# Kernel tuning notes

Hardware: AMD Instinct MI355X
Metric: run time of the kernel (lower is better)

## Reference

```python
import jax, jax.numpy as jnp
from jax import lax
import numpy as np

T, B, I, H, O = 512, 32, 512, 512, 512


def _gru_layer(x_seq, h0, w_ih, w_hh, b_ih, b_hh, reverse):
    """Single-direction GRU layer, PyTorch gate semantics (r,z,n order).
    x_seq: (T,B,in), h0: (B,H). Returns ys:(T,B,H) in original time order, hT:(B,H)."""
    gi = jnp.einsum('tbi,gi->tbg', x_seq, w_ih) + b_ih  # (T,B,3H) input gates precomputed

    def step(h, gi_t):
        gh = h @ w_hh.T + b_hh
        ir, iz, i_n = jnp.split(gi_t, 3, axis=-1)
        hr, hz, hn = jnp.split(gh, 3, axis=-1)
        r = jax.nn.sigmoid(ir + hr)
        z = jax.nn.sigmoid(iz + hz)
        n = jnp.tanh(i_n + r * hn)
        h_new = (1.0 - z) * n + z * h
        return h_new, h_new

    hT, ys = lax.scan(step, h0, gi, reverse=reverse)
    return ys, hT


def setup_inputs() -> dict:
    key = jax.random.key(0)
    ks = jax.random.split(key, 20)
    s = 1.0 / np.sqrt(H)
    u = lambda k, shape: jax.random.uniform(k, shape, jnp.float32, -s, s)
    inp = {
        'x': jax.random.normal(ks[0], (T, B, I), jnp.float32),
        'h': jnp.zeros((4, B, H), jnp.float32),
        # layer 0 (input I), forward/backward
        'w_ih_0f': u(ks[1], (3 * H, I)), 'w_hh_0f': u(ks[2], (3 * H, H)),
        'b_ih_0f': u(ks[3], (3 * H,)),   'b_hh_0f': u(ks[4], (3 * H,)),
        'w_ih_0b': u(ks[5], (3 * H, I)), 'w_hh_0b': u(ks[6], (3 * H, H)),
        'b_ih_0b': u(ks[7], (3 * H,)),   'b_hh_0b': u(ks[8], (3 * H,)),
        # layer 1 (input 2H)
        'w_ih_1f': u(ks[9], (3 * H, 2 * H)), 'w_hh_1f': u(ks[10], (3 * H, H)),
        'b_ih_1f': u(ks[11], (3 * H,)),      'b_hh_1f': u(ks[12], (3 * H,)),
        'w_ih_1b': u(ks[13], (3 * H, 2 * H)), 'w_hh_1b': u(ks[14], (3 * H, H)),
        'b_ih_1b': u(ks[15], (3 * H,)),       'b_hh_1b': u(ks[16], (3 * H,)),
        # final linear: (O, 2H)
        'fc_w': u(ks[17], (O, 2 * H)), 'fc_b': u(ks[18], (O,)),
    }
    return inp


def reference(x, h,
              w_ih_0f, w_hh_0f, b_ih_0f, b_hh_0f,
              w_ih_0b, w_hh_0b, b_ih_0b, b_hh_0b,
              w_ih_1f, w_hh_1f, b_ih_1f, b_hh_1f,
              w_ih_1b, w_hh_1b, b_ih_1b, b_hh_1b,
              fc_w, fc_b):
    # layer 0: h indices 0 (fwd), 1 (bwd)
    y0f, h0f = _gru_layer(x, h[0], w_ih_0f, w_hh_0f, b_ih_0f, b_hh_0f, reverse=False)
    y0b, h0b = _gru_layer(x, h[1], w_ih_0b, w_hh_0b, b_ih_0b, b_hh_0b, reverse=True)
    x1 = jnp.concatenate([y0f, y0b], axis=-1)  # (T,B,2H)
    # layer 1: h indices 2 (fwd), 3 (bwd)
    y1f, h1f = _gru_layer(x1, h[2], w_ih_1f, w_hh_1f, b_ih_1f, b_hh_1f, reverse=False)
    y1b, h1b = _gru_layer(x1, h[3], w_ih_1b, w_hh_1b, b_ih_1b, b_hh_1b, reverse=True)
    out = jnp.concatenate([y1f, y1b], axis=-1)  # (T,B,2H)
    out = jnp.einsum('tbh,oh->tbo', out, fc_w) + fc_b
    h_n = jnp.stack([h0f, h0b, h1f, h1b], axis=0)  # (4,B,H)
    return out, h_n
```

## Files before the change

### kernel.cpp

```cpp
#include <hip/hip_runtime.h>


typedef unsigned short u16;
typedef __attribute__((ext_vector_type(8))) short bf16x8;
typedef __attribute__((ext_vector_type(4))) float f32x4;

__device__ __forceinline__ u16 f2bf(float f) {
  unsigned u = __float_as_uint(f);
  u += 0x7fffu + ((u >> 16) & 1u);
  return (u16)(u >> 16);
}
__device__ __forceinline__ float bf2f(unsigned v) {
  return __uint_as_float(v << 16);
}
__device__ __forceinline__ float frcp(float x) {
  float r;
  asm("v_rcp_f32 %0, %1" : "=v"(r) : "v"(x));
  return r;
}

template<int AUX>
__device__ __forceinline__ void gl_lds16(const void* g, void* l) {
  __builtin_amdgcn_global_load_lds((const __attribute__((address_space(1))) void*)g,
                                   (__attribute__((address_space(3))) void*)l, 16, 0, AUX);
}

__device__ __forceinline__ void st_u64_sc0(void* p, uint2 v) {
  asm volatile("global_store_dwordx2 %0, %1, off sc0" :: "v"(p), "v"(v) : "memory");
}
__device__ __forceinline__ unsigned atom_rd_l2(unsigned* p) {
  unsigned r;
  asm volatile("global_atomic_add %0, %1, %2, off sc0\n\ts_waitcnt vmcnt(0)"
               : "=v"(r) : "v"(p), "v"(0u) : "memory");
  return r;
}
__device__ __forceinline__ void atom_add_l2(unsigned* p, unsigned v) {
  asm volatile("global_atomic_add %0, %1, off" :: "v"(p), "v"(v) : "memory");
}


__global__ void k_zero(unsigned* p, int n) {
  int i = blockIdx.x * blockDim.x + threadIdx.x;
  if (i < n) p[i] = 0u;
}

__global__ void k_cvt(const float* __restrict__ s, u16* __restrict__ d, int n) {
  int i = (blockIdx.x * blockDim.x + threadIdx.x) * 4;
  if (i < n) {
    float4 v = *(const float4*)(s + i);
    unsigned a = (unsigned)f2bf(v.x) | ((unsigned)f2bf(v.y) << 16);
    unsigned b = (unsigned)f2bf(v.z) | ((unsigned)f2bf(v.w) << 16);
    uint2 o; o.x = a; o.y = b;
    *(uint2*)(d + i) = o;
  }
}

__global__ void k_copyf(const float* __restrict__ s, float* __restrict__ d, int n) {
  int i = blockIdx.x * blockDim.x + threadIdx.x;
  if (i < n) d[i] = s[i];
}


template<bool BF16OUT>
__global__ __launch_bounds__(256) void k_gemm(
    const u16* __restrict__ A, const u16* __restrict__ B,
    const float* __restrict__ bias, void* __restrict__ Cv,
    int N, int K)
{
  __shared__ u16 As[128 * 32];
  __shared__ u16 Bs[128 * 32];
  const int tid = threadIdx.x;
  const int w = tid >> 6, l = tid & 63;
  const int bm = blockIdx.x, bn = blockIdx.y;
  const int lj = l & 15, lk = l >> 4;
  const int wm = (w & 1) * 64, wn = (w >> 1) * 64;
  const int srow = l >> 2, scol = (l & 3) * 8;
  f32x4 acc[4][4] = {};
  const u16* Ab = A + (size_t)bm * 128 * K;
  const u16* Bb = B + (size_t)bn * 128 * K;

  for (int kt = 0; kt < K; kt += 32) {
#pragma unroll
    for (int i = 0; i < 2; ++i) {
      int r0 = i * 64 + w * 16;
      gl_lds16<0>(Ab + (size_t)(r0 + srow) * K + kt + scol, &As[r0 * 32]);
      gl_lds16<0>(Bb + (size_t)(r0 + srow) * K + kt + scol, &Bs[r0 * 32]);
    }
    __syncthreads();
    bf16x8 af[4], bf[4];
#pragma unroll
    for (int i = 0; i < 4; ++i) af[i] = *(const bf16x8*)&As[(wm + i * 16 + lj) * 32 + lk * 8];
#pragma unroll
    for (int j = 0; j < 4; ++j) bf[j] = *(const bf16x8*)&Bs[(wn + j * 16 + lj) * 32 + lk * 8];
#pragma unroll
    for (int i = 0; i < 4; ++i)
#pragma unroll
      for (int j = 0; j < 4; ++j)
        acc[i][j] = __builtin_amdgcn_mfma_f32_16x16x32_bf16(af[i], bf[j], acc[i][j], 0, 0, 0);
    __syncthreads();
  }

#pragma unroll
  for (int i = 0; i < 4; ++i)
#pragma unroll
    for (int j = 0; j < 4; ++j) {
      int col = bn * 128 + wn + j * 16 + lj;
      float bv = bias[col];
#pragma unroll
      for (int r2 = 0; r2 < 4; ++r2) {
        int row = bm * 128 + wm + i * 16 + lk * 4 + r2;
        float v = acc[i][j][r2] + bv;
        if (BF16OUT) ((u16*)Cv)[(size_t)row * N + col] = f2bf(v);
        else         ((float*)Cv)[(size_t)row * N + col] = v;
      }
    }
}


#define LSTR 536

__global__ __launch_bounds__(256, 1) void k_gru(
    const u16*  __restrict__ gi,
    const float* __restrict__ whhf,
    const float* __restrict__ whhb,
    const float* __restrict__ bhhf,
    const float* __restrict__ bhhb,
    const float* __restrict__ h0,
    const u16*  __restrict__ hinit,
    u16* __restrict__ y,
    float* __restrict__ hn,
    unsigned* __restrict__ cnt,
    unsigned* __restrict__ elect)
{
  __shared__ u16 hl[2][32 * LSTR];
  __shared__ int sh_role;
  __shared__ int sh_go;
  const int tid = threadIdx.x;

  if (tid == 0) {
    sh_go = -1;
    unsigned xcc;
    asm volatile("s_getreg_b32 %0, hwreg(HW_REG_XCC_ID)" : "=s"(xcc));
    xcc &= 7u;
    unsigned t = __hip_atomic_fetch_add(&elect[xcc], 1u, __ATOMIC_RELAXED,
                                        __HIP_MEMORY_SCOPE_AGENT);
    int role = -1;
    if (t < 16u) {
      if (t == 15u) {
        unsigned expected = 0u;
        __hip_atomic_compare_exchange_strong(&elect[8], &expected, xcc + 1u,
            __ATOMIC_RELAXED, __ATOMIC_RELAXED, __HIP_MEMORY_SCOPE_AGENT);
      }
      unsigned cap = 0;
      for (;;) {
        unsigned wv = __hip_atomic_load(&elect[8], __ATOMIC_RELAXED,
                                        __HIP_MEMORY_SCOPE_AGENT);
        if (wv != 0u) { if (wv == xcc + 1u) role = (int)t; break; }
        if (++cap > (1u << 22)) break;
        __builtin_amdgcn_s_sleep(2);
      }
    }
    sh_role = role;
  }
  __syncthreads();
  const int role = sh_role;
  if (role < 0) return;

  const int w = tid >> 6, l = tid & 63;
  const int dir = w >> 1, p = w & 1;
  const int j0 = role * 32 + p * 16;
  const int lj = l & 15, lk = l >> 4;
  const float* whh = dir ? whhb : whhf;
  const float* bhh = dir ? bhhb : bhhf;
  volatile int* go_v = (volatile int*)&sh_go;

  bf16x8 bfr[3][16];
#pragma unroll
  for (int g = 0; g < 3; ++g) {
    const float* wr = whh + (size_t)(g * 512 + j0 + lj) * 512;
#pragma unroll
    for (int kc = 0; kc < 16; ++kc) {
      const float* s4 = wr + kc * 32 + lk * 8;
      float4 a = *(const float4*)s4;
      float4 b = *(const float4*)(s4 + 4);
      bf16x8 v;
      v[0] = (short)f2bf(a.x); v[1] = (short)f2bf(a.y); v[2] = (short)f2bf(a.z); v[3] = (short)f2bf(a.w);
      v[4] = (short)f2bf(b.x); v[5] = (short)f2bf(b.y); v[6] = (short)f2bf(b.z); v[7] = (short)f2bf(b.w);
      bfr[g][kc] = v;
    }
  }
  f32x4 bbv[3];
#pragma unroll
  for (int g = 0; g < 3; ++g)
    bbv[g] = *(const f32x4*)&bhh[g * 512 + j0 + lk * 4];

  float hreg[2][4];
#pragma unroll
  for (int bt = 0; bt < 2; ++bt) {
    f32x4 hv = *(const f32x4*)&h0[((size_t)dir * 32 + bt * 16 + lj) * 512 + j0 + lk * 4];
#pragma unroll
    for (int r = 0; r < 4; ++r) hreg[bt][r] = hv[r];
  }

  uint2 guc[2][3];
  {
    const int tq0 = dir ? 511 : 0;
#pragma unroll
    for (int bt = 0; bt < 2; ++bt)
#pragma unroll
      for (int g = 0; g < 3; ++g)
        guc[bt][g] = *(const uint2*)(gi + ((size_t)tq0 * 32 + bt * 16 + lj) * 3072
                                     + dir * 1536 + g * 512 + j0 + lk * 4);
  }

  for (int s = 0; s < 512; ++s) {
    const int tq = dir ? (511 - s) : s;

    if (s > 0) {
      if (w == 0) {
        const unsigned target = 4u * (unsigned)s;
        unsigned cap = 0;
        for (;;) {
          unsigned v = 0xFFFFFFFFu;
          if (l < 4) v = atom_rd_l2(cnt + (l << 5));
          if (__all((int)((l < 4) ? (v >= target) : 1))) break;
          if (++cap > (1u << 14)) break;
        }
        if (l == 0) *go_v = s;
      } else {
        unsigned cap = 0;
        while (*go_v < s) { if (++cap > (1u << 20)) break; }
      }
    }

    {
      const u16* src; int rstride, cbase;
      if (s == 0) { src = hinit + (size_t)dir * 32 * 512; rstride = 512; cbase = 0; }
      else { int tp = dir ? (tq + 1) : (tq - 1); src = y + (size_t)tp * 32 * 1024; rstride = 1024; cbase = dir * 512; }
#pragma unroll
      for (int r = 0; r < 16; ++r) {
        int row = p * 16 + r;
        gl_lds16<1>(src + (size_t)row * rstride + cbase + l * 8, &hl[dir][row * LSTR]);
      }
    }
    asm volatile("s_waitcnt vmcnt(0)" ::: "memory");
    __syncthreads();

    uint2 gun[2][3];
    {
      const int sq = (s < 511) ? (s + 1) : 511;
      const int tqn = dir ? (511 - sq) : sq;
#pragma unroll
      for (int bt = 0; bt < 2; ++bt)
#pragma unroll
        for (int g = 0; g < 3; ++g)
          gun[bt][g] = *(const uint2*)(gi + ((size_t)tqn * 32 + bt * 16 + lj) * 3072
                                       + dir * 1536 + g * 512 + j0 + lk * 4);
    }

    f32x4 acc[2][3];
#pragma unroll
    for (int bt = 0; bt < 2; ++bt)
#pragma unroll
      for (int g = 0; g < 3; ++g)
        acc[bt][g] = bbv[g];

#pragma unroll
    for (int kc = 0; kc < 16; ++kc) {
      bf16x8 a0 = *(const bf16x8*)&hl[dir][lj * LSTR + kc * 32 + lk * 8];
      bf16x8 a1 = *(const bf16x8*)&hl[dir][(16 + lj) * LSTR + kc * 32 + lk * 8];
#pragma unroll
      for (int g = 0; g < 3; ++g) {
        acc[0][g] = __builtin_amdgcn_mfma_f32_16x16x32_bf16(bfr[g][kc], a0, acc[0][g], 0, 0, 0);
        acc[1][g] = __builtin_amdgcn_mfma_f32_16x16x32_bf16(bfr[g][kc], a1, acc[1][g], 0, 0, 0);
      }
    }

#pragma unroll
    for (int bt = 0; bt < 2; ++bt) {
      const int b = bt * 16 + lj;
      unsigned q[4];
      float hv[4];
#pragma unroll
      for (int r = 0; r < 4; ++r) {
        unsigned w0 = (r & 1) ? (((const unsigned*)&guc[bt][0])[r >> 1] >> 16)
                              : (((const unsigned*)&guc[bt][0])[r >> 1] & 0xffffu);
        unsigned w1 = (r & 1) ? (((const unsigned*)&guc[bt][1])[r >> 1] >> 16)
                              : (((const unsigned*)&guc[bt][1])[r >> 1] & 0xffffu);
        unsigned w2 = (r & 1) ? (((const unsigned*)&guc[bt][2])[r >> 1] >> 16)
                              : (((const unsigned*)&guc[bt][2])[r >> 1] & 0xffffu);
        float rr = frcp(1.f + __expf(-(bf2f(w0) + acc[bt][0][r])));
        float zz = frcp(1.f + __expf(-(bf2f(w1) + acc[bt][1][r])));
        float nx = bf2f(w2) + rr * acc[bt][2][r];
        float nn = 1.f - 2.f * frcp(1.f + __expf(2.f * nx));
        float h = (1.f - zz) * nn + zz * hreg[bt][r];
        hreg[bt][r] = h;
        hv[r] = h;
        q[r] = (unsigned)f2bf(h);
      }
      uint2 pack; pack.x = q[0] | (q[1] << 16); pack.y = q[2] | (q[3] << 16);
      st_u64_sc0(y + ((size_t)tq * 32 + b) * 1024 + dir * 512 + j0 + lk * 4, pack);
      if (s == 511) {
        float4 o; o.x = hv[0]; o.y = hv[1]; o.z = hv[2]; o.w = hv[3];
        *(float4*)&hn[((size_t)dir * 32 + b) * 512 + j0 + lk * 4] = o;
      }
    }

#pragma unroll
    for (int bt = 0; bt < 2; ++bt)
#pragma unroll
      for (int g = 0; g < 3; ++g)
        guc[bt][g] = gun[bt][g];

    asm volatile("s_waitcnt vmcnt(0)" ::: "memory");
    __syncthreads();
    if (tid == 0) atom_add_l2(cnt + ((role & 3) << 5), 1u);
  }
}


extern "C" void kernel_launch(void* const* d_in, const int* in_sizes, int n_in,
                              void* d_out, int out_size, void* d_ws, size_t ws_size,
                              hipStream_t stream)
{
  const float* x     = (const float*)d_in[0];
  const float* h     = (const float*)d_in[1];
  const float* wih0f = (const float*)d_in[2];
  const float* whh0f = (const float*)d_in[3];
  const float* bih0f = (const float*)d_in[4];
  const float* bhh0f = (const float*)d_in[5];
  const float* wih0b = (const float*)d_in[6];
  const float* whh0b = (const float*)d_in[7];
  const float* bih0b = (const float*)d_in[8];
  const float* bhh0b = (const float*)d_in[9];
  const float* wih1f = (const float*)d_in[10];
  const float* whh1f = (const float*)d_in[11];
  const float* bih1f = (const float*)d_in[12];
  const float* bhh1f = (const float*)d_in[13];
  const float* wih1b = (const float*)d_in[14];
  const float* whh1b = (const float*)d_in[15];
  const float* bih1b = (const float*)d_in[16];
  const float* bhh1b = (const float*)d_in[17];
  const float* fcw   = (const float*)d_in[18];
  const float* fcb   = (const float*)d_in[19];
  (void)in_sizes; (void)n_in; (void)out_size;

  char* ws = (char*)d_ws;
  size_t off = 0;
  auto alloc = [&](size_t bytes) { void* p = ws + off; off += (bytes + 255) & ~(size_t)255; return p; };
  u16*      gi    = (u16*)     alloc(16384ull * 3072 * 2);
  u16*      y0    = (u16*)     alloc(16384ull * 1024 * 2);
  char*     y1r   = (char*)    alloc(16384ull * 1024 * 2);
  u16*      Wfc   = (u16*)     alloc(512ull * 1024 * 2);
  u16*      hinit = (u16*)     alloc(4ull * 32 * 512 * 2);
  float*    bias0 = (float*)   alloc(3072 * 4);
  float*    bias1 = (float*)   alloc(3072 * 4);
  unsigned* sync  = (unsigned*)alloc(512 * 4);
  size_t need = off;

  if (ws_size < need) {
    hipMemsetAsync(d_out, 0, (size_t)out_size * sizeof(float), stream);
    return;
  }

  u16* y1   = (u16*)y1r;
  u16* xb   = (u16*)y1r;
  u16* Wih0 = (u16*)(y1r + 16777216);
  u16* Wih1 = (u16*)(y1r + 16777216 + 3145728);

  float* out = (float*)d_out;
  float* hn  = out + 512ull * 32 * 512;

  k_zero<<<2, 256, 0, stream>>>(sync, 512);
  auto cvt = [&](const float* s, u16* d, int n) {
    k_cvt<<<dim3((n / 4 + 255) / 256), 256, 0, stream>>>(s, d, n);
  };
  cvt(x, xb, 16384 * 512);
  cvt(wih0f, Wih0, 1536 * 512);
  cvt(wih0b, Wih0 + 1536 * 512, 1536 * 512);
  cvt(wih1f, Wih1, 1536 * 1024);
  cvt(wih1b, Wih1 + 1536 * 1024, 1536 * 1024);
  cvt(fcw, Wfc, 512 * 1024);
  cvt(h, hinit, 4 * 32 * 512);
  k_copyf<<<6, 256, 0, stream>>>(bih0f, bias0, 1536);
  k_copyf<<<6, 256, 0, stream>>>(bih0b, bias0 + 1536, 1536);
  k_copyf<<<6, 256, 0, stream>>>(bih1f, bias1, 1536);
  k_copyf<<<6, 256, 0, stream>>>(bih1b, bias1 + 1536, 1536);

  k_gemm<true><<<dim3(128, 24), 256, 0, stream>>>(xb, Wih0, bias0, gi, 3072, 512);
  k_gru<<<128, 256, 0, stream>>>(gi, whh0f, whh0b, bhh0f, bhh0b,
                                 h, hinit, y0, hn, sync, sync + 256);
  k_gemm<true><<<dim3(128, 24), 256, 0, stream>>>(y0, Wih1, bias1, gi, 3072, 1024);
  k_gru<<<128, 256, 0, stream>>>(gi, whh1f, whh1b, bhh1f, bhh1b,
                                 h + 2 * 32 * 512, hinit + 2 * 32 * 512,
                                 y1, hn + 2ull * 32 * 512, sync + 128, sync + 384);
  k_gemm<false><<<dim3(128, 4), 256, 0, stream>>>(y1, Wfc, fcb, out, 512, 1024);
}
```

Baseline: 3.881 ms.

## Split GRU workgroups per direction and replace counters with per-block step flags

Each GRU workgroup now handles a single direction with 128 threads, and 32 workgroups are elected on one XCC instead of 16 workgroups that each carried both directions. The shared atomic counters and the LDS go-flag relay are replaced by per-block step flags written with sc0 stores. Every wave polls the 16 flags of its own direction directly, so forward and backward no longer wait on each other and one atomic handoff hop is removed. The cost is more polling traffic on L2 and twice as many workgroups that must stay co-resident on one XCC.

```diff
diff --git a/kernel.cpp b/kernel.cpp
--- a/kernel.cpp
+++ b/kernel.cpp
@@ -25,6 +25,9 @@
                                    (__attribute__((address_space(3))) void*)l, 16, 0, AUX);
 }
 
+__device__ __forceinline__ void st_u32_sc0(unsigned* p, unsigned v) {
+  asm volatile("global_store_dword %0, %1, off sc0" :: "v"(p), "v"(v) : "memory");
+}
 __device__ __forceinline__ void st_u64_sc0(void* p, uint2 v) {
   asm volatile("global_store_dwordx2 %0, %1, off sc0" :: "v"(p), "v"(v) : "memory");
 }
@@ -33,9 +36,6 @@
   asm volatile("global_atomic_add %0, %1, %2, off sc0\n\ts_waitcnt vmcnt(0)"
                : "=v"(r) : "v"(p), "v"(0u) : "memory");
   return r;
-}
-__device__ __forceinline__ void atom_add_l2(unsigned* p, unsigned v) {
-  asm volatile("global_atomic_add %0, %1, off" :: "v"(p), "v"(v) : "memory");
 }
 
 
@@ -119,7 +119,7 @@
 
 #define LSTR 536
 
-__global__ __launch_bounds__(256, 1) void k_gru(
+__global__ __launch_bounds__(128, 1) void k_gru(
     const u16*  __restrict__ gi,
     const float* __restrict__ whhf,
     const float* __restrict__ whhb,
@@ -129,24 +129,22 @@
     const u16*  __restrict__ hinit,
     u16* __restrict__ y,
     float* __restrict__ hn,
-    unsigned* __restrict__ cnt,
+    unsigned* __restrict__ flags,
     unsigned* __restrict__ elect)
 {
-  __shared__ u16 hl[2][32 * LSTR];
+  __shared__ u16 hl[32 * LSTR];
   __shared__ int sh_role;
-  __shared__ int sh_go;
   const int tid = threadIdx.x;
 
   if (tid == 0) {
-    sh_go = -1;
     unsigned xcc;
     asm volatile("s_getreg_b32 %0, hwreg(HW_REG_XCC_ID)" : "=s"(xcc));
     xcc &= 7u;
     unsigned t = __hip_atomic_fetch_add(&elect[xcc], 1u, __ATOMIC_RELAXED,
                                         __HIP_MEMORY_SCOPE_AGENT);
     int role = -1;
-    if (t < 16u) {
-      if (t == 15u) {
+    if (t < 32u) {
+      if (t == 31u) {
         unsigned expected = 0u;
         __hip_atomic_compare_exchange_strong(&elect[8], &expected, xcc + 1u,
             __ATOMIC_RELAXED, __ATOMIC_RELAXED, __HIP_MEMORY_SCOPE_AGENT);
@@ -156,7 +154,7 @@
         unsigned wv = __hip_atomic_load(&elect[8], __ATOMIC_RELAXED,
                                         __HIP_MEMORY_SCOPE_AGENT);
         if (wv != 0u) { if (wv == xcc + 1u) role = (int)t; break; }
-        if (++cap > (1u << 22)) break;
+        if (++cap > (1u << 18)) break;
         __builtin_amdgcn_s_sleep(2);
       }
     }
@@ -166,13 +164,13 @@
   const int role = sh_role;
   if (role < 0) return;
 
-  const int w = tid >> 6, l = tid & 63;
-  const int dir = w >> 1, p = w & 1;
-  const int j0 = role * 32 + p * 16;
+  const int p = tid >> 6, l = tid & 63;
+  const int dir = role & 1, jg = role >> 1;
+  const int j0 = jg * 32 + p * 16;
   const int lj = l & 15, lk = l >> 4;
   const float* whh = dir ? whhb : whhf;
   const float* bhh = dir ? bhhb : bhhf;
-  volatile int* go_v = (volatile int*)&sh_go;
+  unsigned* fl = flags + dir * 256;
 
   bf16x8 bfr[3][16];
 #pragma unroll
@@ -217,19 +215,13 @@
     const int tq = dir ? (511 - s) : s;
 
     if (s > 0) {
-      if (w == 0) {
-        const unsigned target = 4u * (unsigned)s;
-        unsigned cap = 0;
-        for (;;) {
-          unsigned v = 0xFFFFFFFFu;
-          if (l < 4) v = atom_rd_l2(cnt + (l << 5));
-          if (__all((int)((l < 4) ? (v >= target) : 1))) break;
-          if (++cap > (1u << 14)) break;
-        }
-        if (l == 0) *go_v = s;
-      } else {
-        unsigned cap = 0;
-        while (*go_v < s) { if (++cap > (1u << 20)) break; }
+      const unsigned ss = (unsigned)s;
+      unsigned cap = 0;
+      for (;;) {
+        unsigned v = 0;
+        if (l < 16) v = atom_rd_l2(fl + l * 16 + jg);
+        if (__all((int)((l < 16) ? (v >= ss) : 1))) break;
+        if (++cap > (1u << 16)) break;
       }
     }
 
@@ -240,7 +232,7 @@
 #pragma unroll
       for (int r = 0; r < 16; ++r) {
         int row = p * 16 + r;
-        gl_lds16<1>(src + (size_t)row * rstride + cbase + l * 8, &hl[dir][row * LSTR]);
+        gl_lds16<1>(src + (size_t)row * rstride + cbase + l * 8, &hl[row * LSTR]);
       }
     }
     asm volatile("s_waitcnt vmcnt(0)" ::: "memory");
@@ -267,8 +259,8 @@
 
 #pragma unroll
     for (int kc = 0; kc < 16; ++kc) {
-      bf16x8 a0 = *(const bf16x8*)&hl[dir][lj * LSTR + kc * 32 + lk * 8];
-      bf16x8 a1 = *(const bf16x8*)&hl[dir][(16 + lj) * LSTR + kc * 32 + lk * 8];
+      bf16x8 a0 = *(const bf16x8*)&hl[lj * LSTR + kc * 32 + lk * 8];
+      bf16x8 a1 = *(const bf16x8*)&hl[(16 + lj) * LSTR + kc * 32 + lk * 8];
 #pragma unroll
       for (int g = 0; g < 3; ++g) {
         acc[0][g] = __builtin_amdgcn_mfma_f32_16x16x32_bf16(bfr[g][kc], a0, acc[0][g], 0, 0, 0);
@@ -314,7 +306,8 @@
 
     asm volatile("s_waitcnt vmcnt(0)" ::: "memory");
     __syncthreads();
-    if (tid == 0) atom_add_l2(cnt + ((role & 3) << 5), 1u);
+    if (tid < 16)
+      st_u32_sc0(fl + jg * 16 + tid, (unsigned)(s + 1));
   }
 }
 
@@ -355,7 +348,7 @@
   u16*      hinit = (u16*)     alloc(4ull * 32 * 512 * 2);
   float*    bias0 = (float*)   alloc(3072 * 4);
   float*    bias1 = (float*)   alloc(3072 * 4);
-  unsigned* sync  = (unsigned*)alloc(512 * 4);
+  unsigned* sync  = (unsigned*)alloc(2048 * 4);
   size_t need = off;
 
   if (ws_size < need) {
@@ -371,7 +364,7 @@
   float* out = (float*)d_out;
   float* hn  = out + 512ull * 32 * 512;
 
-  k_zero<<<2, 256, 0, stream>>>(sync, 512);
+  k_zero<<<8, 256, 0, stream>>>(sync, 2048);
   auto cvt = [&](const float* s, u16* d, int n) {
     k_cvt<<<dim3((n / 4 + 255) / 256), 256, 0, stream>>>(s, d, n);
   };
@@ -388,11 +381,11 @@
   k_copyf<<<6, 256, 0, stream>>>(bih1b, bias1 + 1536, 1536);
 
   k_gemm<true><<<dim3(128, 24), 256, 0, stream>>>(xb, Wih0, bias0, gi, 3072, 512);
-  k_gru<<<128, 256, 0, stream>>>(gi, whh0f, whh0b, bhh0f, bhh0b,
-                                 h, hinit, y0, hn, sync, sync + 256);
+  k_gru<<<384, 128, 0, stream>>>(gi, whh0f, whh0b, bhh0f, bhh0b,
+                                 h, hinit, y0, hn, sync, sync + 512);
   k_gemm<true><<<dim3(128, 24), 256, 0, stream>>>(y0, Wih1, bias1, gi, 3072, 1024);
-  k_gru<<<128, 256, 0, stream>>>(gi, whh1f, whh1b, bhh1f, bhh1b,
+  k_gru<<<384, 128, 0, stream>>>(gi, whh1f, whh1b, bhh1f, bhh1b,
                                  h + 2 * 32 * 512, hinit + 2 * 32 * 512,
-                                 y1, hn + 2ull * 32 * 512, sync + 128, sync + 384);
+                                 y1, hn + 2ull * 32 * 512, sync + 1024, sync + 1536);
   k_gemm<false><<<dim3(128, 4), 256, 0, stream>>>(y1, Wfc, fcb, out, 512, 1024);
 }
```

Result: slower. 4.186 ms (+7.9%).

## Overlap next-layer GEMM with GRU recurrence using idle blocks and progress counters

Applied to the files above, without the earlier changes.

The GRU kernel now launches 384 blocks. The 16 elected recurrence blocks publish their per-step progress to a counter array, and the remaining blocks pull GEMM tiles (the layer-1 input projection, or the final FC) from an atomic work queue. Each tile waits until every recurrence block has passed the timesteps that tile covers, both producing its inputs and consuming its gi rows, before it runs. Tiles are ordered from the middle of the sequence outward, because the forward and backward directions both finish those timesteps earliest. This removes the separate serial GEMM launches after each recurrence. The cost is possible L2 and bandwidth contention that could slow the latency-bound recurrence, plus extra cache-coherent stores.

```diff
diff --git a/kernel.cpp b/kernel.cpp
--- a/kernel.cpp
+++ b/kernel.cpp
@@ -25,8 +25,11 @@
                                    (__attribute__((address_space(3))) void*)l, 16, 0, AUX);
 }
 
-__device__ __forceinline__ void st_u64_sc0(void* p, uint2 v) {
-  asm volatile("global_store_dwordx2 %0, %1, off sc0" :: "v"(p), "v"(v) : "memory");
+__device__ __forceinline__ void st_u32_cc(unsigned* p, unsigned v) {
+  asm volatile("global_store_dword %0, %1, off sc0 sc1" :: "v"(p), "v"(v) : "memory");
+}
+__device__ __forceinline__ void st_u64_cc(void* p, uint2 v) {
+  asm volatile("global_store_dwordx2 %0, %1, off sc0 sc1" :: "v"(p), "v"(v) : "memory");
 }
 __device__ __forceinline__ unsigned atom_rd_l2(unsigned* p) {
   unsigned r;
@@ -61,17 +64,12 @@
 }
 
 
-template<bool BF16OUT>
-__global__ __launch_bounds__(256) void k_gemm(
-    const u16* __restrict__ A, const u16* __restrict__ B,
-    const float* __restrict__ bias, void* __restrict__ Cv,
-    int N, int K)
+__device__ __forceinline__ void gemm_tile(
+    const u16* A, const u16* B, const float* bias, void* Cv,
+    int N, int K, int bm, int bn, int bf16out, u16* As, u16* Bs)
 {
-  __shared__ u16 As[128 * 32];
-  __shared__ u16 Bs[128 * 32];
   const int tid = threadIdx.x;
   const int w = tid >> 6, l = tid & 63;
-  const int bm = blockIdx.x, bn = blockIdx.y;
   const int lj = l & 15, lk = l >> 4;
   const int wm = (w & 1) * 64, wn = (w >> 1) * 64;
   const int srow = l >> 2, scol = (l & 3) * 8;
@@ -110,61 +108,105 @@
       for (int r2 = 0; r2 < 4; ++r2) {
         int row = bm * 128 + wm + i * 16 + lk * 4 + r2;
         float v = acc[i][j][r2] + bv;
-        if (BF16OUT) ((u16*)Cv)[(size_t)row * N + col] = f2bf(v);
+        if (bf16out) ((u16*)Cv)[(size_t)row * N + col] = f2bf(v);
         else         ((float*)Cv)[(size_t)row * N + col] = v;
       }
     }
 }
 
+template<bool BF16OUT>
+__global__ __launch_bounds__(256) void k_gemm(
+    const u16* __restrict__ A, const u16* __restrict__ B,
+    const float* __restrict__ bias, void* __restrict__ Cv, int N, int K)
+{
+  __shared__ u16 As[128 * 32];
+  __shared__ u16 Bs[128 * 32];
+  gemm_tile(A, B, bias, Cv, N, K, blockIdx.x, blockIdx.y, BF16OUT ? 1 : 0, As, Bs);
+}
+
 
 #define LSTR 536
 
-__global__ __launch_bounds__(256, 1) void k_gru(
-    const u16*  __restrict__ gi,
+__global__ __launch_bounds__(256, 1) void k_fused(
+    const u16*  gi,
     const float* __restrict__ whhf,
     const float* __restrict__ whhb,
     const float* __restrict__ bhhf,
     const float* __restrict__ bhhb,
     const float* __restrict__ h0,
     const u16*  __restrict__ hinit,
-    u16* __restrict__ y,
+    u16* y,
     float* __restrict__ hn,
     unsigned* __restrict__ cnt,
-    unsigned* __restrict__ elect)
+    unsigned* __restrict__ elect,
+    unsigned* __restrict__ prog,
+    const u16* A2, const u16* B2,
+    const float* bias2, void* C2,
+    int N2, int K2, int ntiles, int nbn, unsigned* __restrict__ queue,
+    int bf16out)
 {
   __shared__ u16 hl[2][32 * LSTR];
-  __shared__ int sh_role;
-  __shared__ int sh_go;
+  __shared__ int sh_role, sh_win, sh_xcc, sh_t;
   const int tid = threadIdx.x;
 
   if (tid == 0) {
-    sh_go = -1;
     unsigned xcc;
     asm volatile("s_getreg_b32 %0, hwreg(HW_REG_XCC_ID)" : "=s"(xcc));
     xcc &= 7u;
     unsigned t = __hip_atomic_fetch_add(&elect[xcc], 1u, __ATOMIC_RELAXED,
                                         __HIP_MEMORY_SCOPE_AGENT);
     int role = -1;
-    if (t < 16u) {
-      if (t == 15u) {
-        unsigned expected = 0u;
-        __hip_atomic_compare_exchange_strong(&elect[8], &expected, xcc + 1u,
-            __ATOMIC_RELAXED, __ATOMIC_RELAXED, __HIP_MEMORY_SCOPE_AGENT);
-      }
+    unsigned wv = 0;
+    if (t == 15u) {
+      unsigned expected = 0u;
+      __hip_atomic_compare_exchange_strong(&elect[8], &expected, xcc + 1u,
+          __ATOMIC_RELAXED, __ATOMIC_RELAXED, __HIP_MEMORY_SCOPE_AGENT);
+    }
+    {
       unsigned cap = 0;
       for (;;) {
-        unsigned wv = __hip_atomic_load(&elect[8], __ATOMIC_RELAXED,
-                                        __HIP_MEMORY_SCOPE_AGENT);
-        if (wv != 0u) { if (wv == xcc + 1u) role = (int)t; break; }
+        wv = __hip_atomic_load(&elect[8], __ATOMIC_RELAXED,
+                               __HIP_MEMORY_SCOPE_AGENT);
+        if (wv != 0u) break;
         if (++cap > (1u << 22)) break;
         __builtin_amdgcn_s_sleep(2);
       }
     }
-    sh_role = role;
+    if (wv == xcc + 1u && t < 16u) role = (int)t;
+    sh_role = role; sh_win = (int)wv; sh_xcc = (int)xcc;
   }
   __syncthreads();
   const int role = sh_role;
-  if (role < 0) return;
+
+  if (role < 0) {
+    if (sh_win != 0 && sh_xcc == sh_win - 1) return;
+    u16* As = &hl[0][0];
+    u16* Bs = &hl[0][4096];
+    const int l = tid & 63;
+    for (;;) {
+      __syncthreads();
+      if (tid == 0)
+        sh_t = (int)__hip_atomic_fetch_add(queue, 1u, __ATOMIC_RELAXED,
+                                           __HIP_MEMORY_SCOPE_AGENT);
+      __syncthreads();
+      const int t = sh_t;
+      if (t >= ntiles) return;
+      const int k = t / nbn, bn = t % nbn;
+      const int bm = (k & 1) ? (63 - (k >> 1)) : (64 + (k >> 1));
+      const unsigned T = (unsigned)max(4 * bm + 4, 512 - 4 * bm);
+      unsigned cap = 0;
+      for (;;) {
+        unsigned v = T;
+        if (l < 16) v = __hip_atomic_load(&prog[l], __ATOMIC_RELAXED,
+                                          __HIP_MEMORY_SCOPE_AGENT);
+        if (__all((int)(v >= T))) break;
+        if (++cap > (1u << 16)) break;
+        __builtin_amdgcn_s_sleep(16);
+      }
+      __syncthreads();
+      gemm_tile(A2, B2, bias2, C2, N2, K2, bm, bn, bf16out, As, Bs);
+    }
+  }
 
   const int w = tid >> 6, l = tid & 63;
   const int dir = w >> 1, p = w & 1;
@@ -172,7 +214,7 @@
   const int lj = l & 15, lk = l >> 4;
   const float* whh = dir ? whhb : whhf;
   const float* bhh = dir ? bhhb : bhhf;
-  volatile int* go_v = (volatile int*)&sh_go;
+  volatile int* go_v = (volatile int*)&sh_t;
 
   bf16x8 bfr[3][16];
 #pragma unroll
@@ -201,6 +243,9 @@
 #pragma unroll
     for (int r = 0; r < 4; ++r) hreg[bt][r] = hv[r];
   }
+
+  if (tid == 0) *go_v = -1;
+  __syncthreads();
 
   uint2 guc[2][3];
   {
@@ -299,7 +344,7 @@
         q[r] = (unsigned)f2bf(h);
       }
       uint2 pack; pack.x = q[0] | (q[1] << 16); pack.y = q[2] | (q[3] << 16);
-      st_u64_sc0(y + ((size_t)tq * 32 + b) * 1024 + dir * 512 + j0 + lk * 4, pack);
+      st_u64_cc(y + ((size_t)tq * 32 + b) * 1024 + dir * 512 + j0 + lk * 4, pack);
       if (s == 511) {
         float4 o; o.x = hv[0]; o.y = hv[1]; o.z = hv[2]; o.w = hv[3];
         *(float4*)&hn[((size_t)dir * 32 + b) * 512 + j0 + lk * 4] = o;
@@ -314,7 +359,11 @@
 
     asm volatile("s_waitcnt vmcnt(0)" ::: "memory");
     __syncthreads();
-    if (tid == 0) atom_add_l2(cnt + ((role & 3) << 5), 1u);
+    if (tid == 0) {
+      atom_add_l2(cnt + ((role & 3) << 5), 1u);
+      if (((s + 1) & 3) == 0)
+        st_u32_cc(&prog[role], (unsigned)(s + 1));
+    }
   }
 }
 
@@ -388,11 +437,16 @@
   k_copyf<<<6, 256, 0, stream>>>(bih1b, bias1 + 1536, 1536);
 
   k_gemm<true><<<dim3(128, 24), 256, 0, stream>>>(xb, Wih0, bias0, gi, 3072, 512);
-  k_gru<<<128, 256, 0, stream>>>(gi, whh0f, whh0b, bhh0f, bhh0b,
-                                 h, hinit, y0, hn, sync, sync + 256);
-  k_gemm<true><<<dim3(128, 24), 256, 0, stream>>>(y0, Wih1, bias1, gi, 3072, 1024);
-  k_gru<<<128, 256, 0, stream>>>(gi, whh1f, whh1b, bhh1f, bhh1b,
-                                 h + 2 * 32 * 512, hinit + 2 * 32 * 512,
-                                 y1, hn + 2ull * 32 * 512, sync + 128, sync + 384);
-  k_gemm<false><<<dim3(128, 4), 256, 0, stream>>>(y1, Wfc, fcb, out, 512, 1024);
-}
+
+  k_fused<<<384, 256, 0, stream>>>(gi, whh0f, whh0b, bhh0f, bhh0b,
+                                   h, hinit, y0, hn,
+                                   sync, sync + 256, sync + 288,
+                                   y0, Wih1, bias1, gi, 3072, 1024, 3072, 24,
+                                   sync + 320, 1);
+  k_fused<<<384, 256, 0, stream>>>(gi, whh1f, whh1b, bhh1f, bhh1b,
+                                   h + 2 * 32 * 512, hinit + 2 * 32 * 512,
+                                   y1, hn + 2ull * 32 * 512,
+                                   sync + 128, sync + 272, sync + 304,
+                                   y1, Wfc, fcb, out, 512, 1024, 512, 4,
+                                   sync + 352, 0);
+}
```

New measurement: 4.039 ms. +4.1%, slower.
